# Kernel tuning notes

Hardware: AMD Instinct MI355X
Metric: run time of the kernel (lower is better)

The kernel has to match this reference:

```python
import jax, jax.numpy as jnp
import numpy as np

N = 2_097_152          # n_transitions = n_envs * buffer_size
GAMMA = 0.99
GAE_LAMBDA = 0.95
CLIP_EPS = 0.2
NORM_ADVANTAGES = True


def setup_inputs() -> dict:
    key = jax.random.key(0)
    ks = jax.random.split(key, 7)
    f = lambda k: jax.random.normal(k, (N, 1), dtype=jnp.float32)
    return {
        "rewards": f(ks[0]),
        "values": f(ks[1]),
        "next_values": f(ks[2]),
        "log_probs": -jnp.abs(f(ks[3])),       # log-probs are <= 0
        "old_log_probs": -jnp.abs(f(ks[4])),
        "terminated": jax.random.randint(ks[5], (N, 1), 0, 2).astype(bool),
        "truncated": jax.random.randint(ks[6], (N, 1), 0, 2).astype(bool),
    }


def reference(rewards, values, next_values, log_probs, old_log_probs,
              terminated, truncated):
    dtype = rewards.dtype
    dones = jnp.logical_or(terminated, truncated)
    not_term = 1.0 - terminated.astype(dtype)          # [N,1]
    not_done = 1.0 - dones.astype(dtype)               # [N,1]

    # TD residuals: delta_n = r_n + gamma * (1 - terminated_n) * V(s'_n) - V(s_n)
    deltas = rewards + GAMMA * not_term * next_values - values   # [N,1]

    # Reverse GAE recurrence (the torch Python for-loop, fused into one scan):
    # adv_n = (1 - done_n) * gamma * lambda * adv_{n+1} + delta_n
    coef = not_done[:, 0] * (GAMMA * GAE_LAMBDA)       # [N]

    def step(adv, cd):
        c, d = cd
        adv = c * adv + d
        return adv, adv

    _, advantages = jax.lax.scan(step, jnp.zeros((), dtype),
                                 (coef, deltas[:, 0]), reverse=True)
    advantages = advantages[:, None]                   # [N,1]

    lambda_returns = advantages + values               # [N,1]

    if NORM_ADVANTAGES:
        # torch .std() is the unbiased (ddof=1) estimator
        adv_n = (advantages - advantages.mean()) / (
            jnp.std(advantages, ddof=1) + 1e-9)
    else:
        adv_n = advantages

    # PPO clipped surrogate, per-sample (the .mean() is a trivial reduction)
    ratio = jnp.exp(log_probs - old_log_probs)
    clamped = jnp.clip(ratio, 1.0 - CLIP_EPS, 1.0 + CLIP_EPS)
    per_sample_actor_loss = -jnp.minimum(ratio * adv_n, clamped * adv_n)

    # [N,3]: normalized advantages, lambda returns, per-sample clipped objective
    return jnp.concatenate([adv_n, lambda_returns, per_sample_actor_loss], axis=1)
```

## Files before the change

### kernel.cpp

```cpp
#include <hip/hip_runtime.h>
#include <stdint.h>

static constexpr int BLOCK = 256;
static constexpr int ITEMS = 8;
static constexpr int CHUNK = BLOCK * ITEMS;
static constexpr int MAXNB = 1024;

#define GAMMA_F 0.99f
static __device__ __forceinline__ float gl_const() { return (float)(0.99 * 0.95); }

__device__ __forceinline__ void compose(float& a1, float& b1, float a2, float b2) {
    b1 = fmaf(a1, b2, b1);
    a1 = a1 * a2;
}

__device__ __forceinline__ int detect_mode(const void* term, int n_elems, int* flg) {
    int t = threadIdx.x;
    if (t == 0) { flg[0] = 0; flg[1] = 0; }
    __syncthreads();
    if (t < 256) {
        const unsigned char* p = (const unsigned char*)term;
        int i0 = 4 * t;
        if (i0 + 3 < n_elems) {
            unsigned b1 = p[i0 + 1], b2 = p[i0 + 2], b3 = p[i0 + 3];
            if (b1) atomicOr(&flg[0], 1);
            if (b2 | b3) atomicOr(&flg[1], 1);
        }
    }
    __syncthreads();
    return flg[0] ? 1 : (flg[1] ? 2 : 0);
}

__device__ __forceinline__ int load_bool1(const void* p, long i, int mode) {
    if (mode == 1) return ((const unsigned char*)p)[i] != 0;
    if (mode == 0) return ((const int*)p)[i] != 0;
    return ((const float*)p)[i] != 0.0f;
}

__device__ __forceinline__ void load_bool8(const void* p, long base, int mode, int* f) {
    if (mode == 1) {
        uint2 q = *(const uint2*)((const unsigned char*)p + base);
        unsigned w[2] = {q.x, q.y};
#pragma unroll
        for (int j = 0; j < 8; ++j) f[j] = (int)((w[j >> 2] >> ((j & 3) * 8)) & 0xffu);
    } else if (mode == 0) {
        const int4* q = (const int4*)((const int*)p + base);
#pragma unroll
        for (int k = 0; k < 2; ++k) {
            int4 v = q[k];
            f[4*k] = v.x; f[4*k+1] = v.y; f[4*k+2] = v.z; f[4*k+3] = v.w;
        }
    } else {
        const float4* q = (const float4*)((const float*)p + base);
#pragma unroll
        for (int k = 0; k < 2; ++k) {
            float4 v = q[k];
            f[4*k] = v.x != 0.f; f[4*k+1] = v.y != 0.f; f[4*k+2] = v.z != 0.f; f[4*k+3] = v.w != 0.f;
        }
    }
}

__device__ __forceinline__ void compute_cd(
    const float* __restrict__ rewards, const float* __restrict__ values,
    const float* __restrict__ next_values, const void* __restrict__ term,
    const void* __restrict__ trunc, int mode, long base, int n,
    float* c, float* d, float* v)
{
    const float GL = gl_const();
    if (base + ITEMS <= n) {
        float r[ITEMS], nv[ITEMS];
        const float4* r4 = (const float4*)(rewards + base);
        const float4* v4 = (const float4*)(values + base);
        const float4* n4 = (const float4*)(next_values + base);
#pragma unroll
        for (int k = 0; k < 2; ++k) {
            float4 a = r4[k]; r[4*k]=a.x; r[4*k+1]=a.y; r[4*k+2]=a.z; r[4*k+3]=a.w;
            float4 b = v4[k]; v[4*k]=b.x; v[4*k+1]=b.y; v[4*k+2]=b.z; v[4*k+3]=b.w;
            float4 q = n4[k]; nv[4*k]=q.x; nv[4*k+1]=q.y; nv[4*k+2]=q.z; nv[4*k+3]=q.w;
        }
        int tm[ITEMS], tr[ITEMS];
        load_bool8(term,  base, mode, tm);
        load_bool8(trunc, base, mode, tr);
#pragma unroll
        for (int j = 0; j < ITEMS; ++j) {
            float nt = tm[j] ? 0.f : 1.f;
            float nd = (tm[j] | tr[j]) ? 0.f : 1.f;
            d[j] = r[j] + GAMMA_F * nt * nv[j] - v[j];
            c[j] = nd * GL;
        }
    } else {
#pragma unroll
        for (int j = 0; j < ITEMS; ++j) {
            long i = base + j;
            if (i < (long)n) {
                int tm = load_bool1(term, i, mode);
                int tr = load_bool1(trunc, i, mode);
                float nt = tm ? 0.f : 1.f;
                float nd = (tm | tr) ? 0.f : 1.f;
                v[j] = values[i];
                d[j] = rewards[i] + GAMMA_F * nt * next_values[i] - v[j];
                c[j] = nd * GL;
            } else { c[j] = 1.f; d[j] = 0.f; v[j] = 0.f; }
        }
    }
}

__global__ __launch_bounds__(BLOCK) void k1_agg(
    const float* __restrict__ rewards, const float* __restrict__ values,
    const float* __restrict__ next_values, const void* __restrict__ term,
    const void* __restrict__ trunc, float2* __restrict__ blockAgg,
    float2* __restrict__ E2, float4* __restrict__ bs4, float* __restrict__ bs1,
    int n)
{
    __shared__ int flg[2];
    __shared__ float wA[4], wB[4];
    __shared__ float red[4][5];

    const int t = threadIdx.x;
    const int lane = t & 63, w = t >> 6;
    const int bid = blockIdx.x;
    const int mode = detect_mode(term, n, flg);
    const long base = (long)bid * CHUNK + (long)t * ITEMS;

    float c[ITEMS], d[ITEMS], v[ITEMS];
    compute_cd(rewards, values, next_values, term, trunc, mode, base, n, c, d, v);

    float a = 1.f, b = 0.f;
#pragma unroll
    for (int j = ITEMS - 1; j >= 0; --j) { b = fmaf(c[j], b, d[j]); a *= c[j]; }

#pragma unroll
    for (int dd = 1; dd < 64; dd <<= 1) {
        float ra = __shfl_down(a, dd, 64);
        float rb = __shfl_down(b, dd, 64);
        if (lane + dd < 64) { b = fmaf(a, rb, b); a *= ra; }
    }
    if (lane == 0) { wA[w] = a; wB[w] = b; }
    float ea = __shfl_down(a, 1, 64);
    float eb = __shfl_down(b, 1, 64);
    if (lane == 63) { ea = 1.f; eb = 0.f; }
    __syncthreads();
    for (int ww = w + 1; ww < 4; ++ww) compose(ea, eb, wA[ww], wB[ww]);
    if (t == 0) {
        float Aa = wA[0], Ab = wB[0];
        for (int ww = 1; ww < 4; ++ww) compose(Aa, Ab, wA[ww], wB[ww]);
        blockAgg[bid] = make_float2(Aa, Ab);
    }
    E2[(long)bid * BLOCK + t] = make_float2(ea, eb);

    float p = ea, q = eb;
    float sP = 0.f, sQ = 0.f, sP2 = 0.f, sPQ = 0.f, sQ2 = 0.f;
#pragma unroll
    for (int j = ITEMS - 1; j >= 0; --j) {
        p = c[j] * p;
        q = fmaf(c[j], q, d[j]);
        if (base + j < (long)n) {
            sP += p; sQ += q; sP2 += p*p; sPQ += p*q; sQ2 += q*q;
        }
    }
#pragma unroll
    for (int dd = 32; dd > 0; dd >>= 1) {
        sP  += __shfl_down(sP,  dd, 64);
        sQ  += __shfl_down(sQ,  dd, 64);
        sP2 += __shfl_down(sP2, dd, 64);
        sPQ += __shfl_down(sPQ, dd, 64);
        sQ2 += __shfl_down(sQ2, dd, 64);
    }
    if (lane == 0) { red[w][0]=sP; red[w][1]=sQ; red[w][2]=sP2; red[w][3]=sPQ; red[w][4]=sQ2; }
    __syncthreads();
    if (t == 0) {
        float m0=0,m1=0,m2=0,m3=0,m4=0;
        for (int ww = 0; ww < 4; ++ww) { m0+=red[ww][0]; m1+=red[ww][1]; m2+=red[ww][2]; m3+=red[ww][3]; m4+=red[ww][4]; }
        bs4[bid] = make_float4(m0, m1, m2, m3);
        bs1[bid] = m4;
    }
}

__global__ __launch_bounds__(BLOCK) void k3_final(
    const float* __restrict__ rewards, const float* __restrict__ values,
    const float* __restrict__ next_values, const void* __restrict__ term,
    const void* __restrict__ trunc, const float* __restrict__ lp,
    const float* __restrict__ olp, const float2* __restrict__ E2,
    const float2* __restrict__ blockAgg, const float4* __restrict__ bs4,
    const float* __restrict__ bs1, float* __restrict__ out, int n, int nb)
{
    __shared__ int flg[2];
    __shared__ float sA[BLOCK], sB[BLOCK];
    __shared__ float sS[MAXNB];
    __shared__ double dS[BLOCK], dS2[BLOCK];
    __shared__ float statMean, statInv;

    const int t = threadIdx.x;
    const int bid = blockIdx.x;
    const int mode = detect_mode(term, n, flg);
    const long base = (long)bid * CHUNK + (long)t * ITEMS;

    float c[ITEMS], d[ITEMS], v[ITEMS];
    compute_cd(rewards, values, next_values, term, trunc, mode, base, n, c, d, v);
    float2 e = E2[(long)bid * BLOCK + t];

    float la[4], lb[4];
#pragma unroll
    for (int j = 0; j < 4; ++j) {
        int i = 4 * t + j;
        if (i < nb) { float2 f = blockAgg[i]; la[j] = f.x; lb[j] = f.y; }
        else        { la[j] = 1.f; lb[j] = 0.f; }
    }
    float a = 1.f, b = 0.f;
#pragma unroll
    for (int j = 3; j >= 0; --j) { b = fmaf(la[j], b, lb[j]); a *= la[j]; }
    sA[t] = a; sB[t] = b;
    __syncthreads();
    for (int dd = 1; dd < BLOCK; dd <<= 1) {
        float ra = 1.f, rb = 0.f;
        if (t + dd < BLOCK) { ra = sA[t + dd]; rb = sB[t + dd]; }
        __syncthreads();
        b = fmaf(a, rb, b);
        a *= ra;
        sA[t] = a; sB[t] = b;
        __syncthreads();
    }
    float x = (t + 1 < BLOCK) ? sB[t + 1] : 0.f;
    double ds = 0.0, ds2 = 0.0;
#pragma unroll
    for (int j = 3; j >= 0; --j) {
        int i = 4 * t + j;
        if (i < nb) {
            sS[i] = x;
            float4 s4 = bs4[i];
            double xd = (double)x;
            ds  += (double)s4.x * xd + (double)s4.y;
            ds2 += (double)s4.z * xd * xd + 2.0 * (double)s4.w * xd + (double)bs1[i];
        }
        x = fmaf(la[j], x, lb[j]);
    }
    dS[t] = ds; dS2[t] = ds2;
    __syncthreads();
    for (int dd = BLOCK / 2; dd > 0; dd >>= 1) {
        if (t < dd) { dS[t] += dS[t + dd]; dS2[t] += dS2[t + dd]; }
        __syncthreads();
    }
    if (t == 0) {
        double sum = dS[0], sumsq = dS2[0];
        double mean = sum / (double)n;
        double var = (sumsq - sum * sum / (double)n) / (double)(n - 1);
        if (var < 0.0) var = 0.0;
        statMean = (float)mean;
        statInv  = 1.0f / ((float)sqrt(var) + 1e-9f);
    }
    __syncthreads();

    float xx = fmaf(e.x, sS[bid], e.y);
    float adv[ITEMS];
#pragma unroll
    for (int j = ITEMS - 1; j >= 0; --j) {
        xx = fmaf(c[j], xx, d[j]);
        adv[j] = xx;
    }
    const float mean = statMean;
    const float inv  = statInv;
    if (base + ITEMS <= n) {
        float l[ITEMS], o[ITEMS];
        const float4* l4 = (const float4*)(lp + base);
        const float4* o4 = (const float4*)(olp + base);
#pragma unroll
        for (int k = 0; k < 2; ++k) {
            float4 q = l4[k]; l[4*k]=q.x; l[4*k+1]=q.y; l[4*k+2]=q.z; l[4*k+3]=q.w;
            float4 w = o4[k]; o[4*k]=w.x; o[4*k+1]=w.y; o[4*k+2]=w.z; o[4*k+3]=w.w;
        }
        float buf[3 * ITEMS];
#pragma unroll
        for (int j = 0; j < ITEMS; ++j) {
            float an = (adv[j] - mean) * inv;
            float ratio = expf(l[j] - o[j]);
            float cl = fminf(fmaxf(ratio, 0.8f), 1.2f);
            buf[3*j]     = an;
            buf[3*j + 1] = adv[j] + v[j];
            buf[3*j + 2] = -fminf(ratio * an, cl * an);
        }
        float4* dst = (float4*)(out + 3 * base);
#pragma unroll
        for (int k = 0; k < 6; ++k)
            dst[k] = make_float4(buf[4*k], buf[4*k+1], buf[4*k+2], buf[4*k+3]);
    } else {
        for (int j = 0; j < ITEMS; ++j) {
            long i = base + j;
            if (i < (long)n) {
                float an = (adv[j] - mean) * inv;
                float ratio = expf(lp[i] - olp[i]);
                float cl = fminf(fmaxf(ratio, 0.8f), 1.2f);
                out[3*i]     = an;
                out[3*i + 1] = adv[j] + v[j];
                out[3*i + 2] = -fminf(ratio * an, cl * an);
            }
        }
    }
}

extern "C" void kernel_launch(void* const* d_in, const int* in_sizes, int n_in,
                              void* d_out, int out_size, void* d_ws, size_t ws_size,
                              hipStream_t stream) {
    const float* rewards     = (const float*)d_in[0];
    const float* values      = (const float*)d_in[1];
    const float* next_values = (const float*)d_in[2];
    const float* lp          = (const float*)d_in[3];
    const float* olp         = (const float*)d_in[4];
    const void*  term        = d_in[5];
    const void*  trunc       = d_in[6];
    float* out = (float*)d_out;
    int n = in_sizes[0];
    int nb = (n + CHUNK - 1) / CHUNK;

    char* ws = (char*)d_ws;
    float2* blockAgg = (float2*)ws;
    float4* bs4      = (float4*)(ws + MAXNB * 8);
    float*  bs1      = (float*) (ws + MAXNB * 8 + MAXNB * 16);
    float2* E2       = (float2*)(ws + MAXNB * 8 + MAXNB * 16 + MAXNB * 4 + 256);

    k1_agg <<<nb, BLOCK, 0, stream>>>(rewards, values, next_values, term, trunc,
                                      blockAgg, E2, bs4, bs1, n);
    k3_final<<<nb, BLOCK, 0, stream>>>(rewards, values, next_values, term, trunc,
                                       lp, olp, E2, blockAgg, bs4, bs1, out, n, nb);
}
```

Measured before the change: 130.0 us.

## Fuse two-pass GAE scan into one cooperative kernel with grid sync

Replaces the two-kernel pipeline (block aggregate pass, then final pass that reloads inputs) with a single cooperative kernel. Per-thread c/d/v values stay in registers across a grid-wide sync. Every block then redundantly scans the block aggregates and reduces the mean/variance statistics. This avoids rereading rewards, values, next_values and the masks in a second kernel and removes one launch, but it depends on all 1024 blocks being co-resident and adds a grid barrier plus a redundant per-block scan.

```diff
diff --git a/kernel.cpp b/kernel.cpp
--- a/kernel.cpp
+++ b/kernel.cpp
@@ -1,5 +1,8 @@
 #include <hip/hip_runtime.h>
+#include <hip/hip_cooperative_groups.h>
 #include <stdint.h>
+
+namespace cg = cooperative_groups;
 
 static constexpr int BLOCK = 256;
 static constexpr int ITEMS = 8;
@@ -101,6 +104,189 @@
                 d[j] = rewards[i] + GAMMA_F * nt * next_values[i] - v[j];
                 c[j] = nd * GL;
             } else { c[j] = 1.f; d[j] = 0.f; v[j] = 0.f; }
+        }
+    }
+}
+
+__global__ __launch_bounds__(BLOCK, 4) void k_fused(
+    const float* __restrict__ rewards, const float* __restrict__ values,
+    const float* __restrict__ next_values, const float* __restrict__ lp,
+    const float* __restrict__ olp, const void* __restrict__ term,
+    const void* __restrict__ trunc, float2* __restrict__ blockAgg,
+    float4* __restrict__ bs4, float* __restrict__ bs1,
+    float* __restrict__ out, int n, int nb)
+{
+    __shared__ int flg[2];
+    __shared__ float wA[4], wB[4];
+    __shared__ float red[4][5];
+    __shared__ float sA[BLOCK], sB[BLOCK];
+    __shared__ float sS[MAXNB];
+    __shared__ double dS[BLOCK], dS2[BLOCK];
+    __shared__ float statMean, statInv;
+
+    const int t = threadIdx.x;
+    const int lane = t & 63, w = t >> 6;
+    const int bid = blockIdx.x;
+    const int mode = detect_mode(term, n, flg);
+    const long base = (long)bid * CHUNK + (long)t * ITEMS;
+
+    float c[ITEMS], d[ITEMS], v[ITEMS];
+    compute_cd(rewards, values, next_values, term, trunc, mode, base, n, c, d, v);
+
+    float a = 1.f, b = 0.f;
+#pragma unroll
+    for (int j = ITEMS - 1; j >= 0; --j) { b = fmaf(c[j], b, d[j]); a *= c[j]; }
+
+#pragma unroll
+    for (int dd = 1; dd < 64; dd <<= 1) {
+        float ra = __shfl_down(a, dd, 64);
+        float rb = __shfl_down(b, dd, 64);
+        if (lane + dd < 64) { b = fmaf(a, rb, b); a *= ra; }
+    }
+    if (lane == 0) { wA[w] = a; wB[w] = b; }
+    float ea = __shfl_down(a, 1, 64);
+    float eb = __shfl_down(b, 1, 64);
+    if (lane == 63) { ea = 1.f; eb = 0.f; }
+    __syncthreads();
+    for (int ww = w + 1; ww < 4; ++ww) compose(ea, eb, wA[ww], wB[ww]);
+    if (t == 0) {
+        float Aa = wA[0], Ab = wB[0];
+        for (int ww = 1; ww < 4; ++ww) compose(Aa, Ab, wA[ww], wB[ww]);
+        blockAgg[bid] = make_float2(Aa, Ab);
+    }
+
+    {
+        float p = ea, q = eb;
+        float sP = 0.f, sQ = 0.f, sP2 = 0.f, sPQ = 0.f, sQ2 = 0.f;
+#pragma unroll
+        for (int j = ITEMS - 1; j >= 0; --j) {
+            p = c[j] * p;
+            q = fmaf(c[j], q, d[j]);
+            if (base + j < (long)n) {
+                sP += p; sQ += q; sP2 += p*p; sPQ += p*q; sQ2 += q*q;
+            }
+        }
+#pragma unroll
+        for (int dd = 32; dd > 0; dd >>= 1) {
+            sP  += __shfl_down(sP,  dd, 64);
+            sQ  += __shfl_down(sQ,  dd, 64);
+            sP2 += __shfl_down(sP2, dd, 64);
+            sPQ += __shfl_down(sPQ, dd, 64);
+            sQ2 += __shfl_down(sQ2, dd, 64);
+        }
+        if (lane == 0) { red[w][0]=sP; red[w][1]=sQ; red[w][2]=sP2; red[w][3]=sPQ; red[w][4]=sQ2; }
+        __syncthreads();
+        if (t == 0) {
+            float m0=0,m1=0,m2=0,m3=0,m4=0;
+            for (int ww = 0; ww < 4; ++ww) { m0+=red[ww][0]; m1+=red[ww][1]; m2+=red[ww][2]; m3+=red[ww][3]; m4+=red[ww][4]; }
+            bs4[bid] = make_float4(m0, m1, m2, m3);
+            bs1[bid] = m4;
+        }
+    }
+
+    const bool full = (base + ITEMS <= n);
+    float l[ITEMS], o[ITEMS];
+    if (full) {
+        const float4* l4 = (const float4*)(lp + base);
+        const float4* o4 = (const float4*)(olp + base);
+#pragma unroll
+        for (int k = 0; k < 2; ++k) {
+            float4 q = l4[k]; l[4*k]=q.x; l[4*k+1]=q.y; l[4*k+2]=q.z; l[4*k+3]=q.w;
+            float4 ww = o4[k]; o[4*k]=ww.x; o[4*k+1]=ww.y; o[4*k+2]=ww.z; o[4*k+3]=ww.w;
+        }
+    }
+
+    __threadfence();
+    cg::this_grid().sync();
+
+    float la[4], lb[4];
+#pragma unroll
+    for (int j = 0; j < 4; ++j) {
+        int i = 4 * t + j;
+        if (i < nb) { float2 f = blockAgg[i]; la[j] = f.x; lb[j] = f.y; }
+        else        { la[j] = 1.f; lb[j] = 0.f; }
+    }
+    a = 1.f; b = 0.f;
+#pragma unroll
+    for (int j = 3; j >= 0; --j) { b = fmaf(la[j], b, lb[j]); a *= la[j]; }
+    sA[t] = a; sB[t] = b;
+    __syncthreads();
+    for (int dd = 1; dd < BLOCK; dd <<= 1) {
+        float ra = 1.f, rb = 0.f;
+        if (t + dd < BLOCK) { ra = sA[t + dd]; rb = sB[t + dd]; }
+        __syncthreads();
+        b = fmaf(a, rb, b);
+        a *= ra;
+        sA[t] = a; sB[t] = b;
+        __syncthreads();
+    }
+    {
+        float x = (t + 1 < BLOCK) ? sB[t + 1] : 0.f;
+        double ds = 0.0, ds2 = 0.0;
+#pragma unroll
+        for (int j = 3; j >= 0; --j) {
+            int i = 4 * t + j;
+            if (i < nb) {
+                sS[i] = x;
+                float4 s4 = bs4[i];
+                double xd = (double)x;
+                ds  += (double)s4.x * xd + (double)s4.y;
+                ds2 += (double)s4.z * xd * xd + 2.0 * (double)s4.w * xd + (double)bs1[i];
+            }
+            x = fmaf(la[j], x, lb[j]);
+        }
+        dS[t] = ds; dS2[t] = ds2;
+    }
+    __syncthreads();
+    for (int dd = BLOCK / 2; dd > 0; dd >>= 1) {
+        if (t < dd) { dS[t] += dS[t + dd]; dS2[t] += dS2[t + dd]; }
+        __syncthreads();
+    }
+    if (t == 0) {
+        double sum = dS[0], sumsq = dS2[0];
+        double mean = sum / (double)n;
+        double var = (sumsq - sum * sum / (double)n) / (double)(n - 1);
+        if (var < 0.0) var = 0.0;
+        statMean = (float)mean;
+        statInv  = 1.0f / ((float)sqrt(var) + 1e-9f);
+    }
+    __syncthreads();
+
+    float xx = fmaf(ea, sS[bid], eb);
+    float adv[ITEMS];
+#pragma unroll
+    for (int j = ITEMS - 1; j >= 0; --j) {
+        xx = fmaf(c[j], xx, d[j]);
+        adv[j] = xx;
+    }
+    const float mean = statMean;
+    const float inv  = statInv;
+    if (full) {
+        float buf[3 * ITEMS];
+#pragma unroll
+        for (int j = 0; j < ITEMS; ++j) {
+            float an = (adv[j] - mean) * inv;
+            float ratio = expf(l[j] - o[j]);
+            float cl = fminf(fmaxf(ratio, 0.8f), 1.2f);
+            buf[3*j]     = an;
+            buf[3*j + 1] = adv[j] + v[j];
+            buf[3*j + 2] = -fminf(ratio * an, cl * an);
+        }
+        float4* dst = (float4*)(out + 3 * base);
+#pragma unroll
+        for (int k = 0; k < 6; ++k)
+            dst[k] = make_float4(buf[4*k], buf[4*k+1], buf[4*k+2], buf[4*k+3]);
+    } else {
+        for (int j = 0; j < ITEMS; ++j) {
+            long i = base + j;
+            if (i < (long)n) {
+                float an = (adv[j] - mean) * inv;
+                float ratio = expf(lp[i] - olp[i]);
+                float cl = fminf(fmaxf(ratio, 0.8f), 1.2f);
+                out[3*i]     = an;
+                out[3*i + 1] = adv[j] + v[j];
+                out[3*i + 2] = -fminf(ratio * an, cl * an);
+            }
         }
     }
 }
@@ -317,8 +503,18 @@
     float*  bs1      = (float*) (ws + MAXNB * 8 + MAXNB * 16);
     float2* E2       = (float2*)(ws + MAXNB * 8 + MAXNB * 16 + MAXNB * 4 + 256);
 
-    k1_agg <<<nb, BLOCK, 0, stream>>>(rewards, values, next_values, term, trunc,
-                                      blockAgg, E2, bs4, bs1, n);
-    k3_final<<<nb, BLOCK, 0, stream>>>(rewards, values, next_values, term, trunc,
-                                       lp, olp, E2, blockAgg, bs4, bs1, out, n, nb);
-}
+    void* kargs[] = {
+        (void*)&rewards, (void*)&values, (void*)&next_values, (void*)&lp,
+        (void*)&olp, (void*)&term, (void*)&trunc, (void*)&blockAgg,
+        (void*)&bs4, (void*)&bs1, (void*)&out, (void*)&n, (void*)&nb
+    };
+    hipError_t err = hipLaunchCooperativeKernel(
+        (const void*)k_fused, dim3((unsigned)nb), dim3(BLOCK), kargs, 0, stream);
+
+    if (err != hipSuccess) {
+        k1_agg <<<nb, BLOCK, 0, stream>>>(rewards, values, next_values, term, trunc,
+                                          blockAgg, E2, bs4, bs1, n);
+        k3_final<<<nb, BLOCK, 0, stream>>>(rewards, values, next_values, term, trunc,
+                                           lp, olp, E2, blockAgg, bs4, bs1, out, n, nb);
+    }
+}
```

Result: slower. 331.2 us (+154.8%).
